# Kernel optimization log

Hardware: AMD Instinct MI355X
Metric: run time of the kernel (lower is better)

Reference implementation:

```python
import jax, jax.numpy as jnp
import numpy as np

N = 100000
E = 1600000
IN_C, HID_C, OUT_C = 64, 64, 16


def setup_inputs() -> dict:
    key = jax.random.key(0)
    k1, k2, k3, k4, k5 = jax.random.split(key, 5)
    x = jax.random.normal(k1, (N, IN_C), dtype=jnp.float32)
    edge_index = jax.random.randint(k2, (2, E), 0, N, dtype=jnp.int64)
    # Glorot-style init like PyG GCNConv
    W1 = jax.random.normal(k3, (IN_C, HID_C), dtype=jnp.float32) * (1.0 / np.sqrt(IN_C))
    b1 = jnp.zeros((HID_C,), dtype=jnp.float32)
    W2 = jax.random.normal(k4, (HID_C, OUT_C), dtype=jnp.float32) * (1.0 / np.sqrt(HID_C))
    b2 = jnp.zeros((OUT_C,), dtype=jnp.float32)
    return {"x": x, "edge_index": edge_index, "W1": W1, "b1": b1, "W2": W2, "b2": b2}


def _gcn_conv(h, src, dst, norm, W, b, n_nodes):
    # h: [N, F_in] -> linear transform first (PyG order), then normalized aggregation
    h = h @ W  # [N, F_out]
    msgs = h[src] * norm[:, None]          # gather + scale, [E+N, F_out]
    out = jax.ops.segment_sum(msgs, dst, num_segments=n_nodes)  # scatter-add
    return out + b


def reference(x, edge_index, W1, b1, W2, b2):
    n = x.shape[0]
    loop = jnp.arange(n, dtype=edge_index.dtype)
    src = jnp.concatenate([edge_index[0], loop])  # add self-loops
    dst = jnp.concatenate([edge_index[1], loop])
    # symmetric normalization D^{-1/2} (A+I) D^{-1/2}
    deg = jax.ops.segment_sum(jnp.ones_like(dst, dtype=x.dtype), dst, num_segments=n)
    dinv = jnp.where(deg > 0, jax.lax.rsqrt(deg), 0.0)
    norm = dinv[src] * dinv[dst]  # [E+N]

    h = jax.nn.relu(_gcn_conv(x, src, dst, norm, W1, b1, n))
    # dropout is identity in eval mode
    return _gcn_conv(h, src, dst, norm, W2, b2, n)
```

## Files before the change

kernel.cpp:

```cpp
#include <hip/hip_runtime.h>


namespace {
constexpr int BLK = 256;
constexpr int NPB = 256;
constexpr int PCHUNK = 8192;
constexpr int STRIDE = 5120;
constexpr int CPAD = 32;

__device__ inline float bf2f(unsigned short h) {
    union { unsigned u; float f; } v; v.u = (unsigned)h << 16; return v.f;
}
__device__ inline unsigned short f2bf(float f) {
    union { float f; unsigned u; } v; v.f = f;
    unsigned r = (v.u + 0x7FFFu + ((v.u >> 16) & 1u)) >> 16;
    return (unsigned short)r;
}
__device__ inline unsigned pack2bf(float a, float b) {
    return (unsigned)f2bf(a) | ((unsigned)f2bf(b) << 16);
}
__device__ inline int sel4(int s0, int s1, int s2, int s3, int q) {
    int sa = (q & 1) ? s1 : s0;
    int sb = (q & 1) ? s3 : s2;
    return (q & 2) ? sb : sa;
}

__device__ inline float gather8(const unsigned short* __restrict__ hhat,
                                const int* __restrict__ ssrc, int base, int lane) {
    int s0 = ssrc[base + 0], s1 = ssrc[base + 1];
    int s2 = ssrc[base + 2], s3 = ssrc[base + 3];
    int s4 = ssrc[base + 4], s5 = ssrc[base + 5];
    int s6 = ssrc[base + 6], s7 = ssrc[base + 7];
    float v0 = bf2f(hhat[((size_t)s0 << 6) + lane]);
    float v1 = bf2f(hhat[((size_t)s1 << 6) + lane]);
    float v2 = bf2f(hhat[((size_t)s2 << 6) + lane]);
    float v3 = bf2f(hhat[((size_t)s3 << 6) + lane]);
    float v4 = bf2f(hhat[((size_t)s4 << 6) + lane]);
    float v5 = bf2f(hhat[((size_t)s5 << 6) + lane]);
    float v6 = bf2f(hhat[((size_t)s6 << 6) + lane]);
    float v7 = bf2f(hhat[((size_t)s7 << 6) + lane]);
    return ((v0 + v1) + (v2 + v3)) + ((v4 + v5) + (v6 + v7));
}
__device__ inline float gather4(const unsigned short* __restrict__ hhat,
                                const int* __restrict__ ssrc, int base, int lane) {
    int s0 = ssrc[base + 0], s1 = ssrc[base + 1];
    int s2 = ssrc[base + 2], s3 = ssrc[base + 3];
    float v0 = bf2f(hhat[((size_t)s0 << 6) + lane]);
    float v1 = bf2f(hhat[((size_t)s1 << 6) + lane]);
    float v2 = bf2f(hhat[((size_t)s2 << 6) + lane]);
    float v3 = bf2f(hhat[((size_t)s3 << 6) + lane]);
    return (v0 + v1) + (v2 + v3);
}

__global__ __launch_bounds__(BLK) void k_part(const int* __restrict__ src,
                                              const int* __restrict__ dst,
                                              int* __restrict__ bcnt,
                                              unsigned* __restrict__ packed,
                                              int e, int nb) {
    __shared__ int hist[1024];
    __shared__ int base[1024];
    int t = threadIdx.x;
    int chunk0 = blockIdx.x * PCHUNK;
    if (chunk0 >= e) return;
    int lim = min(PCHUNK, e - chunk0);
    int lim4 = lim >> 2;
    for (int i = t; i < nb; i += BLK) hist[i] = 0;
    __syncthreads();
    const int4* d4 = (const int4*)(dst + chunk0);
    for (int i = t; i < lim4; i += BLK) {
        int4 d = d4[i];
        atomicAdd(&hist[d.x >> 8], 1);
        atomicAdd(&hist[d.y >> 8], 1);
        atomicAdd(&hist[d.z >> 8], 1);
        atomicAdd(&hist[d.w >> 8], 1);
    }
    for (int i = (lim4 << 2) + t; i < lim; i += BLK)
        atomicAdd(&hist[dst[chunk0 + i] >> 8], 1);
    __syncthreads();
    for (int i = t; i < nb; i += BLK) {
        int c = hist[i];
        base[i] = c ? (i * STRIDE + atomicAdd(&bcnt[i * CPAD], c)) : 0;
        hist[i] = 0;
    }
    __syncthreads();
    const int4* s4 = (const int4*)(src + chunk0);
    for (int i = t; i < lim4; i += BLK) {
        int4 d = d4[i];
        int4 s = s4[i];
        int b0 = d.x >> 8, b1 = d.y >> 8, b2 = d.z >> 8, b3 = d.w >> 8;
        int r0 = atomicAdd(&hist[b0], 1);
        packed[base[b0] + r0] = ((unsigned)s.x << 8) | (unsigned)(d.x & 255);
        int r1 = atomicAdd(&hist[b1], 1);
        packed[base[b1] + r1] = ((unsigned)s.y << 8) | (unsigned)(d.y & 255);
        int r2 = atomicAdd(&hist[b2], 1);
        packed[base[b2] + r2] = ((unsigned)s.z << 8) | (unsigned)(d.z & 255);
        int r3 = atomicAdd(&hist[b3], 1);
        packed[base[b3] + r3] = ((unsigned)s.w << 8) | (unsigned)(d.w & 255);
    }
    for (int i = (lim4 << 2) + t; i < lim; i += BLK) {
        int d = dst[chunk0 + i];
        int b = d >> 8;
        int r = atomicAdd(&hist[b], 1);
        packed[base[b] + r] = ((unsigned)src[chunk0 + i] << 8) | (unsigned)(d & 255);
    }
}

__global__ __launch_bounds__(BLK) void k_meta(const unsigned* __restrict__ packed,
                                              const int* __restrict__ bcnt,
                                              int* __restrict__ rowbeg,
                                              int* __restrict__ rowcnt,
                                              float* __restrict__ dinv, int n) {
    __shared__ int cnt[NPB];
    __shared__ int offs[NPB];
    int b = blockIdx.x;
    int t = threadIdx.x;
    int regionBase = b * STRIDE;
    int ecnt = bcnt[b * CPAD];
    cnt[t] = 0;
    __syncthreads();
    int e4 = ecnt >> 2;
    const uint4* p4 = (const uint4*)(packed + regionBase);
    for (int i = t; i < e4; i += BLK) {
        uint4 p = p4[i];
        atomicAdd(&cnt[p.x & 255u], 1);
        atomicAdd(&cnt[p.y & 255u], 1);
        atomicAdd(&cnt[p.z & 255u], 1);
        atomicAdd(&cnt[p.w & 255u], 1);
    }
    for (int i = (e4 << 2) + t; i < ecnt; i += BLK)
        atomicAdd(&cnt[packed[regionBase + i] & 255u], 1);
    __syncthreads();
    int v = cnt[t];
    offs[t] = v;
    __syncthreads();
    for (int off = 1; off < NPB; off <<= 1) {
        int x = (t >= off) ? offs[t - off] : 0;
        __syncthreads();
        offs[t] += x;
        __syncthreads();
    }
    int node = (b << 8) + t;
    if (node < n) {
        rowbeg[node] = regionBase + offs[t] - v;
        rowcnt[node] = v;
        dinv[node] = rsqrtf((float)(v + 1));
    }
}

union SMemU {
    int cnt[NPB];
    float W[64 * 64];
};

__global__ __launch_bounds__(BLK) void k_sortgemm(
    const unsigned* __restrict__ packed, const int* __restrict__ bcnt,
    const int* __restrict__ rowbeg, int* __restrict__ ssrc, int nsort, int n,
    const float* __restrict__ x, const float* __restrict__ W1,
    const float* __restrict__ dinv, unsigned short* __restrict__ hhat,
    int ntiles) {
    __shared__ SMemU sm;
    int t = threadIdx.x;
    if ((int)blockIdx.x < nsort) {
        int bid = blockIdx.x;
        int b = bid >> 1;
        int hf = bid & 1;
        int regionBase = b * STRIDE;
        int ecnt = bcnt[b * CPAD];
        int node = (b << 8) + t;
        sm.cnt[t] = (node < n) ? rowbeg[node] : 0;
        __syncthreads();
        int lo = hf << 7, hi = lo + 128;
        int e4 = ecnt >> 2;
        const uint4* p4 = (const uint4*)(packed + regionBase);
        for (int i = t; i < e4; i += BLK) {
            uint4 pp = p4[i];
            unsigned a[4] = {pp.x, pp.y, pp.z, pp.w};
            #pragma unroll
            for (int k = 0; k < 4; ++k) {
                int dl = (int)(a[k] & 255u);
                if (dl >= lo && dl < hi) {
                    int pos = atomicAdd(&sm.cnt[dl], 1);
                    ssrc[pos] = (int)(a[k] >> 8);
                }
            }
        }
        for (int i = (e4 << 2) + t; i < ecnt; i += BLK) {
            unsigned p = packed[regionBase + i];
            int dl = (int)(p & 255u);
            if (dl >= lo && dl < hi) {
                int pos = atomicAdd(&sm.cnt[dl], 1);
                ssrc[pos] = (int)(p >> 8);
            }
        }
    } else {
        #pragma unroll
        for (int i = 0; i < 16; ++i) sm.W[t + BLK * i] = W1[t + BLK * i];
        __syncthreads();
        const int cg = t & 3;
        const int ng = t >> 2;
        const float* Wc = sm.W + cg * 16;
        const int g1grid = gridDim.x - nsort;

        for (int tile = blockIdx.x - nsort; tile < ntiles; tile += g1grid) {
            const int node0 = tile * 256 + ng * 4;
            int nd[4];
            #pragma unroll
            for (int i = 0; i < 4; ++i) {
                int vv = node0 + i;
                nd[i] = (vv < n) ? vv : (n - 1);
            }
            float4 acc[4][4];
            #pragma unroll
            for (int i = 0; i < 4; ++i)
                #pragma unroll
                for (int c = 0; c < 4; ++c) acc[i][c] = make_float4(0.f, 0.f, 0.f, 0.f);

            for (int k4 = 0; k4 < 16; ++k4) {
                float4 xv[4];
                #pragma unroll
                for (int i = 0; i < 4; ++i)
                    xv[i] = ((const float4*)(x + (size_t)nd[i] * 64))[k4];
                #pragma unroll
                for (int kk = 0; kk < 4; ++kk) {
                    const float4* wr = (const float4*)(Wc + (k4 * 4 + kk) * 64);
                    float4 w0 = wr[0], w1 = wr[1], w2 = wr[2], w3 = wr[3];
                    #pragma unroll
                    for (int i = 0; i < 4; ++i) {
                        float xa[4] = {xv[i].x, xv[i].y, xv[i].z, xv[i].w};
                        float xs = xa[kk];
                        acc[i][0].x = fmaf(xs, w0.x, acc[i][0].x);
                        acc[i][0].y = fmaf(xs, w0.y, acc[i][0].y);
                        acc[i][0].z = fmaf(xs, w0.z, acc[i][0].z);
                        acc[i][0].w = fmaf(xs, w0.w, acc[i][0].w);
                        acc[i][1].x = fmaf(xs, w1.x, acc[i][1].x);
                        acc[i][1].y = fmaf(xs, w1.y, acc[i][1].y);
                        acc[i][1].z = fmaf(xs, w1.z, acc[i][1].z);
                        acc[i][1].w = fmaf(xs, w1.w, acc[i][1].w);
                        acc[i][2].x = fmaf(xs, w2.x, acc[i][2].x);
                        acc[i][2].y = fmaf(xs, w2.y, acc[i][2].y);
                        acc[i][2].z = fmaf(xs, w2.z, acc[i][2].z);
                        acc[i][2].w = fmaf(xs, w2.w, acc[i][2].w);
                        acc[i][3].x = fmaf(xs, w3.x, acc[i][3].x);
                        acc[i][3].y = fmaf(xs, w3.y, acc[i][3].y);
                        acc[i][3].z = fmaf(xs, w3.z, acc[i][3].z);
                        acc[i][3].w = fmaf(xs, w3.w, acc[i][3].w);
                    }
                }
            }
            #pragma unroll
            for (int i = 0; i < 4; ++i) {
                int vv = node0 + i;
                if (vv < n) {
                    float d = dinv[vv];
                    unsigned u0 = pack2bf(acc[i][0].x * d, acc[i][0].y * d);
                    unsigned u1 = pack2bf(acc[i][0].z * d, acc[i][0].w * d);
                    unsigned u2 = pack2bf(acc[i][1].x * d, acc[i][1].y * d);
                    unsigned u3 = pack2bf(acc[i][1].z * d, acc[i][1].w * d);
                    unsigned u4 = pack2bf(acc[i][2].x * d, acc[i][2].y * d);
                    unsigned u5 = pack2bf(acc[i][2].z * d, acc[i][2].w * d);
                    unsigned u6 = pack2bf(acc[i][3].x * d, acc[i][3].y * d);
                    unsigned u7 = pack2bf(acc[i][3].z * d, acc[i][3].w * d);
                    uint4* dstp = (uint4*)(hhat + (size_t)vv * 64 + cg * 16);
                    dstp[0] = make_uint4(u0, u1, u2, u3);
                    dstp[1] = make_uint4(u4, u5, u6, u7);
                }
            }
        }
    }
}


__global__ __launch_bounds__(BLK) void k_agg1(const unsigned short* __restrict__ hhat,
                                              const int* __restrict__ rowbeg,
                                              const int* __restrict__ rowcnt,
                                              const int* __restrict__ ssrc,
                                              const float* __restrict__ dinv,
                                              const float* __restrict__ b1,
                                              const float* __restrict__ W2,
                                              unsigned short* __restrict__ h2hat, int n) {
    int pair = __builtin_amdgcn_readfirstlane(
        (int)((blockIdx.x * BLK + threadIdx.x) >> 6));
    int lane = threadIdx.x & 63;
    int wid0 = pair << 1;
    if (wid0 >= n) return;
    int wid1 = wid0 + 1;
    bool has1 = (wid1 < n);
    const int g = lane >> 4;
    const int j = lane & 15;
    float w2r[16];
    #pragma unroll
    for (int k = 0; k < 16; ++k) w2r[k] = W2[(g * 16 + k) * 16 + j];

    int beg0 = rowbeg[wid0], cnt0 = rowcnt[wid0];
    int beg1 = 0, cnt1 = 0;
    if (has1) { beg1 = rowbeg[wid1]; cnt1 = rowcnt[wid1]; }
    float a0 = bf2f(hhat[((size_t)wid0 << 6) + lane]);
    float a1 = 0.f;
    if (has1) a1 = bf2f(hhat[((size_t)wid1 << 6) + lane]);
    int e0 = 0, e1 = 0;
    while (e0 + 8 <= cnt0 && e1 + 8 <= cnt1) {
        float r0 = gather8(hhat, ssrc, beg0 + e0, lane);
        float r1 = gather8(hhat, ssrc, beg1 + e1, lane);
        a0 += r0;
        a1 += r1;
        e0 += 8; e1 += 8;
    }
    for (; e0 + 8 <= cnt0; e0 += 8) a0 += gather8(hhat, ssrc, beg0 + e0, lane);
    for (; e1 + 8 <= cnt1; e1 += 8) a1 += gather8(hhat, ssrc, beg1 + e1, lane);
    if (e0 + 4 <= cnt0) { a0 += gather4(hhat, ssrc, beg0 + e0, lane); e0 += 4; }
    if (e1 + 4 <= cnt1) { a1 += gather4(hhat, ssrc, beg1 + e1, lane); e1 += 4; }
    for (; e0 < cnt0; ++e0) a0 += bf2f(hhat[((size_t)ssrc[beg0 + e0] << 6) + lane]);
    for (; e1 < cnt1; ++e1) a1 += bf2f(hhat[((size_t)ssrc[beg1 + e1] << 6) + lane]);

    {
        float dv = dinv[wid0];
        float h = fmaxf(fmaf(dv, a0, b1[lane]), 0.f);
        float part = 0.f;
        #pragma unroll
        for (int k = 0; k < 16; ++k)
            part = fmaf(__shfl(h, g * 16 + k, 64), w2r[k], part);
        part += __shfl_xor(part, 16, 64);
        part += __shfl_xor(part, 32, 64);
        if (g == 0) h2hat[(size_t)wid0 * 16 + j] = f2bf(part * dv);
    }
    if (has1) {
        float dv = dinv[wid1];
        float h = fmaxf(fmaf(dv, a1, b1[lane]), 0.f);
        float part = 0.f;
        #pragma unroll
        for (int k = 0; k < 16; ++k)
            part = fmaf(__shfl(h, g * 16 + k, 64), w2r[k], part);
        part += __shfl_xor(part, 16, 64);
        part += __shfl_xor(part, 32, 64);
        if (g == 0) h2hat[(size_t)wid1 * 16 + j] = f2bf(part * dv);
    }
}

__global__ __launch_bounds__(BLK) void k_agg2(const unsigned short* __restrict__ h2,
                                              const int* __restrict__ rowbeg,
                                              const int* __restrict__ rowcnt,
                                              const int* __restrict__ ssrc,
                                              const float* __restrict__ dinv,
                                              const float* __restrict__ b2,
                                              float* __restrict__ out, int n) {
    int pair = __builtin_amdgcn_readfirstlane(
        (int)((blockIdx.x * BLK + threadIdx.x) >> 6));
    int lane = threadIdx.x & 63;
    int w0 = pair << 1;
    if (w0 >= n) return;
    int w1 = w0 + 1;
    bool has1 = (w1 < n);
    int q = lane >> 4;
    int c = lane & 15;
    int beg0 = rowbeg[w0], cnt0 = rowcnt[w0];
    int beg1 = 0, cnt1 = 0;
    if (has1) { beg1 = rowbeg[w1]; cnt1 = rowcnt[w1]; }
    float a0 = 0.f, a1 = 0.f;
    int e0 = 0, e1 = 0;
    while (e0 + 8 <= cnt0 && e1 + 8 <= cnt1) {
        int p0 = beg0 + e0, p1 = beg1 + e1;
        int x0 = ssrc[p0 + 0], x1 = ssrc[p0 + 1], x2 = ssrc[p0 + 2], x3 = ssrc[p0 + 3];
        int x4 = ssrc[p0 + 4], x5 = ssrc[p0 + 5], x6 = ssrc[p0 + 6], x7 = ssrc[p0 + 7];
        int y0 = ssrc[p1 + 0], y1 = ssrc[p1 + 1], y2 = ssrc[p1 + 2], y3 = ssrc[p1 + 3];
        int y4 = ssrc[p1 + 4], y5 = ssrc[p1 + 5], y6 = ssrc[p1 + 6], y7 = ssrc[p1 + 7];
        int sA0 = sel4(x0, x1, x2, x3, q), sB0 = sel4(x4, x5, x6, x7, q);
        int sA1 = sel4(y0, y1, y2, y3, q), sB1 = sel4(y4, y5, y6, y7, q);
        float vA0 = bf2f(h2[((size_t)sA0 << 4) + c]);
        float vB0 = bf2f(h2[((size_t)sB0 << 4) + c]);
        float vA1 = bf2f(h2[((size_t)sA1 << 4) + c]);
        float vB1 = bf2f(h2[((size_t)sB1 << 4) + c]);
        a0 += vA0 + vB0;
        a1 += vA1 + vB1;
        e0 += 8; e1 += 8;
    }
    for (; e0 + 8 <= cnt0; e0 += 8) {
        int p0 = beg0 + e0;
        int x0 = ssrc[p0 + 0], x1 = ssrc[p0 + 1], x2 = ssrc[p0 + 2], x3 = ssrc[p0 + 3];
        int x4 = ssrc[p0 + 4], x5 = ssrc[p0 + 5], x6 = ssrc[p0 + 6], x7 = ssrc[p0 + 7];
        int sA = sel4(x0, x1, x2, x3, q), sB = sel4(x4, x5, x6, x7, q);
        a0 += bf2f(h2[((size_t)sA << 4) + c]) + bf2f(h2[((size_t)sB << 4) + c]);
    }
    if (e0 + 4 <= cnt0) {
        int p0 = beg0 + e0;
        int x0 = ssrc[p0 + 0], x1 = ssrc[p0 + 1], x2 = ssrc[p0 + 2], x3 = ssrc[p0 + 3];
        a0 += bf2f(h2[((size_t)sel4(x0, x1, x2, x3, q) << 4) + c]);
        e0 += 4;
    }
    if (e0 + q < cnt0)
        a0 += bf2f(h2[((size_t)ssrc[beg0 + e0 + q] << 4) + c]);
    for (; e1 + 8 <= cnt1; e1 += 8) {
        int p1 = beg1 + e1;
        int y0 = ssrc[p1 + 0], y1 = ssrc[p1 + 1], y2 = ssrc[p1 + 2], y3 = ssrc[p1 + 3];
        int y4 = ssrc[p1 + 4], y5 = ssrc[p1 + 5], y6 = ssrc[p1 + 6], y7 = ssrc[p1 + 7];
        int sA = sel4(y0, y1, y2, y3, q), sB = sel4(y4, y5, y6, y7, q);
        a1 += bf2f(h2[((size_t)sA << 4) + c]) + bf2f(h2[((size_t)sB << 4) + c]);
    }
    if (has1 && e1 + 4 <= cnt1) {
        int p1 = beg1 + e1;
        int y0 = ssrc[p1 + 0], y1 = ssrc[p1 + 1], y2 = ssrc[p1 + 2], y3 = ssrc[p1 + 3];
        a1 += bf2f(h2[((size_t)sel4(y0, y1, y2, y3, q) << 4) + c]);
        e1 += 4;
    }
    if (has1 && e1 + q < cnt1)
        a1 += bf2f(h2[((size_t)ssrc[beg1 + e1 + q] << 4) + c]);

    a0 += __shfl_xor(a0, 16, 64);
    a0 += __shfl_xor(a0, 32, 64);
    a1 += __shfl_xor(a1, 16, 64);
    a1 += __shfl_xor(a1, 32, 64);
    if (q == 0) {
        float self0 = bf2f(h2[((size_t)w0 << 4) + c]);
        out[((size_t)w0 << 4) + c] = fmaf(dinv[w0], a0 + self0, b2[c]);
        if (has1) {
            float self1 = bf2f(h2[((size_t)w1 << 4) + c]);
            out[((size_t)w1 << 4) + c] = fmaf(dinv[w1], a1 + self1, b2[c]);
        }
    }
}

}

extern "C" void kernel_launch(void* const* d_in, const int* in_sizes, int n_in,
                              void* d_out, int out_size, void* d_ws, size_t ws_size,
                              hipStream_t stream) {
    const float* x  = (const float*)d_in[0];
    const int*   ei = (const int*)d_in[1];
    const float* W1 = (const float*)d_in[2];
    const float* b1 = (const float*)d_in[3];
    const float* W2 = (const float*)d_in[4];
    const float* b2 = (const float*)d_in[5];
    float* out = (float*)d_out;

    const int N = in_sizes[0] / 64;
    const int E = in_sizes[1] / 2;
    const int* src = ei;
    const int* dst = ei + E;
    const int nb = (N + NPB - 1) / NPB;

    char* ws = (char*)d_ws;
    size_t off = 0;
    auto alloc = [&](size_t bytes) -> char* {
        char* p = ws + off;
        off = (off + bytes + 255) & ~(size_t)255;
        return p;
    };
    int*            bcnt   = (int*)alloc((size_t)1024 * CPAD * 4);
    int*            rowbeg = (int*)alloc((size_t)N * 4);
    int*            rowcnt = (int*)alloc((size_t)N * 4);
    float*          dinv   = (float*)alloc((size_t)N * 4);
    unsigned*       packed = (unsigned*)alloc((size_t)nb * STRIDE * 4);
    int*            ssrc   = (int*)alloc((size_t)nb * STRIDE * 4);
    unsigned short* hhat   = (unsigned short*)alloc((size_t)N * 64 * 2);
    unsigned short* h2hat  = (unsigned short*)alloc((size_t)N * 16 * 2);

    const int ntiles = (N + 255) / 256;
    const int g1grid = (ntiles < 1024) ? ntiles : 1024;
    const int nchunks = (E + PCHUNK - 1) / PCHUNK;
    const int npairs = (N + 1) / 2;
    const int nb_p = (int)(((long long)npairs * 64 + BLK - 1) / BLK);
    const int nsort = nb * 2;

    hipMemsetAsync(bcnt, 0, (size_t)nb * CPAD * 4, stream);
    k_part<<<nchunks, BLK, 0, stream>>>(src, dst, bcnt, packed, E, nb);
    k_meta<<<nb, BLK, 0, stream>>>(packed, bcnt, rowbeg, rowcnt, dinv, N);
    k_sortgemm<<<nsort + g1grid, BLK, 0, stream>>>(packed, bcnt, rowbeg, ssrc,
                                                   nsort, N, x, W1, dinv, hhat,
                                                   ntiles);
    k_agg1<<<nb_p, BLK, 0, stream>>>(hhat, rowbeg, rowcnt, ssrc, dinv, b1, W2,
                                     h2hat, N);
    k_agg2<<<nb_p, BLK, 0, stream>>>(h2hat, rowbeg, rowcnt, ssrc, dinv, b2, out, N);
}
```

Before: 201.1 us.

## Move layer-1 GEMM into partition kernel, defer dinv scaling to scatter kernel

Fuses the x@W1 GEMM blocks into the edge-partition launch instead of the sort launch, writing unscaled fp32 results to a new buffer. A separate pass in the scatter kernel then applies dinv and packs to bf16 once degrees are known. The aim is to overlap the GEMM with partitioning. In exchange it adds a full fp32 intermediate write and read.

```diff
diff --git a/kernel.cpp b/kernel.cpp
--- a/kernel.cpp
+++ b/kernel.cpp
@@ -52,145 +52,62 @@
     return (v0 + v1) + (v2 + v3);
 }
 
-__global__ __launch_bounds__(BLK) void k_part(const int* __restrict__ src,
-                                              const int* __restrict__ dst,
-                                              int* __restrict__ bcnt,
-                                              unsigned* __restrict__ packed,
-                                              int e, int nb) {
-    __shared__ int hist[1024];
-    __shared__ int base[1024];
-    int t = threadIdx.x;
-    int chunk0 = blockIdx.x * PCHUNK;
-    if (chunk0 >= e) return;
-    int lim = min(PCHUNK, e - chunk0);
-    int lim4 = lim >> 2;
-    for (int i = t; i < nb; i += BLK) hist[i] = 0;
-    __syncthreads();
-    const int4* d4 = (const int4*)(dst + chunk0);
-    for (int i = t; i < lim4; i += BLK) {
-        int4 d = d4[i];
-        atomicAdd(&hist[d.x >> 8], 1);
-        atomicAdd(&hist[d.y >> 8], 1);
-        atomicAdd(&hist[d.z >> 8], 1);
-        atomicAdd(&hist[d.w >> 8], 1);
-    }
-    for (int i = (lim4 << 2) + t; i < lim; i += BLK)
-        atomicAdd(&hist[dst[chunk0 + i] >> 8], 1);
-    __syncthreads();
-    for (int i = t; i < nb; i += BLK) {
-        int c = hist[i];
-        base[i] = c ? (i * STRIDE + atomicAdd(&bcnt[i * CPAD], c)) : 0;
-        hist[i] = 0;
-    }
-    __syncthreads();
-    const int4* s4 = (const int4*)(src + chunk0);
-    for (int i = t; i < lim4; i += BLK) {
-        int4 d = d4[i];
-        int4 s = s4[i];
-        int b0 = d.x >> 8, b1 = d.y >> 8, b2 = d.z >> 8, b3 = d.w >> 8;
-        int r0 = atomicAdd(&hist[b0], 1);
-        packed[base[b0] + r0] = ((unsigned)s.x << 8) | (unsigned)(d.x & 255);
-        int r1 = atomicAdd(&hist[b1], 1);
-        packed[base[b1] + r1] = ((unsigned)s.y << 8) | (unsigned)(d.y & 255);
-        int r2 = atomicAdd(&hist[b2], 1);
-        packed[base[b2] + r2] = ((unsigned)s.z << 8) | (unsigned)(d.z & 255);
-        int r3 = atomicAdd(&hist[b3], 1);
-        packed[base[b3] + r3] = ((unsigned)s.w << 8) | (unsigned)(d.w & 255);
-    }
-    for (int i = (lim4 << 2) + t; i < lim; i += BLK) {
-        int d = dst[chunk0 + i];
-        int b = d >> 8;
-        int r = atomicAdd(&hist[b], 1);
-        packed[base[b] + r] = ((unsigned)src[chunk0 + i] << 8) | (unsigned)(d & 255);
-    }
-}
-
-__global__ __launch_bounds__(BLK) void k_meta(const unsigned* __restrict__ packed,
-                                              const int* __restrict__ bcnt,
-                                              int* __restrict__ rowbeg,
-                                              int* __restrict__ rowcnt,
-                                              float* __restrict__ dinv, int n) {
-    __shared__ int cnt[NPB];
-    __shared__ int offs[NPB];
-    int b = blockIdx.x;
-    int t = threadIdx.x;
-    int regionBase = b * STRIDE;
-    int ecnt = bcnt[b * CPAD];
-    cnt[t] = 0;
-    __syncthreads();
-    int e4 = ecnt >> 2;
-    const uint4* p4 = (const uint4*)(packed + regionBase);
-    for (int i = t; i < e4; i += BLK) {
-        uint4 p = p4[i];
-        atomicAdd(&cnt[p.x & 255u], 1);
-        atomicAdd(&cnt[p.y & 255u], 1);
-        atomicAdd(&cnt[p.z & 255u], 1);
-        atomicAdd(&cnt[p.w & 255u], 1);
-    }
-    for (int i = (e4 << 2) + t; i < ecnt; i += BLK)
-        atomicAdd(&cnt[packed[regionBase + i] & 255u], 1);
-    __syncthreads();
-    int v = cnt[t];
-    offs[t] = v;
-    __syncthreads();
-    for (int off = 1; off < NPB; off <<= 1) {
-        int x = (t >= off) ? offs[t - off] : 0;
-        __syncthreads();
-        offs[t] += x;
-        __syncthreads();
-    }
-    int node = (b << 8) + t;
-    if (node < n) {
-        rowbeg[node] = regionBase + offs[t] - v;
-        rowcnt[node] = v;
-        dinv[node] = rsqrtf((float)(v + 1));
-    }
-}
-
-union SMemU {
-    int cnt[NPB];
+union SMemP {
+    struct { int hist[1024]; int base[1024]; } p;
     float W[64 * 64];
 };
 
-__global__ __launch_bounds__(BLK) void k_sortgemm(
-    const unsigned* __restrict__ packed, const int* __restrict__ bcnt,
-    const int* __restrict__ rowbeg, int* __restrict__ ssrc, int nsort, int n,
-    const float* __restrict__ x, const float* __restrict__ W1,
-    const float* __restrict__ dinv, unsigned short* __restrict__ hhat,
-    int ntiles) {
-    __shared__ SMemU sm;
+__global__ __launch_bounds__(BLK) void k_partgemm(
+    const int* __restrict__ src, const int* __restrict__ dst,
+    int* __restrict__ bcnt, unsigned* __restrict__ packed, int e, int nb,
+    int nchunks, const float* __restrict__ x, const float* __restrict__ W1,
+    float* __restrict__ h32, int n, int ntiles) {
+    __shared__ SMemP sm;
     int t = threadIdx.x;
-    if ((int)blockIdx.x < nsort) {
-        int bid = blockIdx.x;
-        int b = bid >> 1;
-        int hf = bid & 1;
-        int regionBase = b * STRIDE;
-        int ecnt = bcnt[b * CPAD];
-        int node = (b << 8) + t;
-        sm.cnt[t] = (node < n) ? rowbeg[node] : 0;
-        __syncthreads();
-        int lo = hf << 7, hi = lo + 128;
-        int e4 = ecnt >> 2;
-        const uint4* p4 = (const uint4*)(packed + regionBase);
-        for (int i = t; i < e4; i += BLK) {
-            uint4 pp = p4[i];
-            unsigned a[4] = {pp.x, pp.y, pp.z, pp.w};
-            #pragma unroll
-            for (int k = 0; k < 4; ++k) {
-                int dl = (int)(a[k] & 255u);
-                if (dl >= lo && dl < hi) {
-                    int pos = atomicAdd(&sm.cnt[dl], 1);
-                    ssrc[pos] = (int)(a[k] >> 8);
-                }
-            }
-        }
-        for (int i = (e4 << 2) + t; i < ecnt; i += BLK) {
-            unsigned p = packed[regionBase + i];
-            int dl = (int)(p & 255u);
-            if (dl >= lo && dl < hi) {
-                int pos = atomicAdd(&sm.cnt[dl], 1);
-                ssrc[pos] = (int)(p >> 8);
-            }
+    if ((int)blockIdx.x < nchunks) {
+        int chunk0 = blockIdx.x * PCHUNK;
+        if (chunk0 >= e) return;
+        int lim = min(PCHUNK, e - chunk0);
+        int lim4 = lim >> 2;
+        for (int i = t; i < nb; i += BLK) sm.p.hist[i] = 0;
+        __syncthreads();
+        const int4* d4 = (const int4*)(dst + chunk0);
+        for (int i = t; i < lim4; i += BLK) {
+            int4 d = d4[i];
+            atomicAdd(&sm.p.hist[d.x >> 8], 1);
+            atomicAdd(&sm.p.hist[d.y >> 8], 1);
+            atomicAdd(&sm.p.hist[d.z >> 8], 1);
+            atomicAdd(&sm.p.hist[d.w >> 8], 1);
+        }
+        for (int i = (lim4 << 2) + t; i < lim; i += BLK)
+            atomicAdd(&sm.p.hist[dst[chunk0 + i] >> 8], 1);
+        __syncthreads();
+        for (int i = t; i < nb; i += BLK) {
+            int c = sm.p.hist[i];
+            sm.p.base[i] = c ? (i * STRIDE + atomicAdd(&bcnt[i * CPAD], c)) : 0;
+            sm.p.hist[i] = 0;
+        }
+        __syncthreads();
+        const int4* s4 = (const int4*)(src + chunk0);
+        for (int i = t; i < lim4; i += BLK) {
+            int4 d = d4[i];
+            int4 s = s4[i];
+            int b0 = d.x >> 8, b1 = d.y >> 8, b2 = d.z >> 8, b3 = d.w >> 8;
+            int r0 = atomicAdd(&sm.p.hist[b0], 1);
+            packed[sm.p.base[b0] + r0] = ((unsigned)s.x << 8) | (unsigned)(d.x & 255);
+            int r1 = atomicAdd(&sm.p.hist[b1], 1);
+            packed[sm.p.base[b1] + r1] = ((unsigned)s.y << 8) | (unsigned)(d.y & 255);
+            int r2 = atomicAdd(&sm.p.hist[b2], 1);
+            packed[sm.p.base[b2] + r2] = ((unsigned)s.z << 8) | (unsigned)(d.z & 255);
+            int r3 = atomicAdd(&sm.p.hist[b3], 1);
+            packed[sm.p.base[b3] + r3] = ((unsigned)s.w << 8) | (unsigned)(d.w & 255);
+        }
+        for (int i = (lim4 << 2) + t; i < lim; i += BLK) {
+            int d = dst[chunk0 + i];
+            int b = d >> 8;
+            int r = atomicAdd(&sm.p.hist[b], 1);
+            packed[sm.p.base[b] + r] =
+                ((unsigned)src[chunk0 + i] << 8) | (unsigned)(d & 255);
         }
     } else {
         #pragma unroll
@@ -199,9 +116,9 @@
         const int cg = t & 3;
         const int ng = t >> 2;
         const float* Wc = sm.W + cg * 16;
-        const int g1grid = gridDim.x - nsort;
-
-        for (int tile = blockIdx.x - nsort; tile < ntiles; tile += g1grid) {
+        const int g1grid = gridDim.x - nchunks;
+
+        for (int tile = blockIdx.x - nchunks; tile < ntiles; tile += g1grid) {
             const int node0 = tile * 256 + ng * 4;
             int nd[4];
             #pragma unroll
@@ -251,19 +168,111 @@
             for (int i = 0; i < 4; ++i) {
                 int vv = node0 + i;
                 if (vv < n) {
-                    float d = dinv[vv];
-                    unsigned u0 = pack2bf(acc[i][0].x * d, acc[i][0].y * d);
-                    unsigned u1 = pack2bf(acc[i][0].z * d, acc[i][0].w * d);
-                    unsigned u2 = pack2bf(acc[i][1].x * d, acc[i][1].y * d);
-                    unsigned u3 = pack2bf(acc[i][1].z * d, acc[i][1].w * d);
-                    unsigned u4 = pack2bf(acc[i][2].x * d, acc[i][2].y * d);
-                    unsigned u5 = pack2bf(acc[i][2].z * d, acc[i][2].w * d);
-                    unsigned u6 = pack2bf(acc[i][3].x * d, acc[i][3].y * d);
-                    unsigned u7 = pack2bf(acc[i][3].z * d, acc[i][3].w * d);
-                    uint4* dstp = (uint4*)(hhat + (size_t)vv * 64 + cg * 16);
-                    dstp[0] = make_uint4(u0, u1, u2, u3);
-                    dstp[1] = make_uint4(u4, u5, u6, u7);
+                    float4* dstp = (float4*)(h32 + (size_t)vv * 64 + cg * 16);
+                    dstp[0] = acc[i][0];
+                    dstp[1] = acc[i][1];
+                    dstp[2] = acc[i][2];
+                    dstp[3] = acc[i][3];
                 }
+            }
+        }
+    }
+}
+
+__global__ __launch_bounds__(BLK) void k_meta(const unsigned* __restrict__ packed,
+                                              const int* __restrict__ bcnt,
+                                              int* __restrict__ rowbeg,
+                                              int* __restrict__ rowcnt,
+                                              float* __restrict__ dinv, int n) {
+    __shared__ int cnt[NPB];
+    __shared__ int offs[NPB];
+    int b = blockIdx.x;
+    int t = threadIdx.x;
+    int regionBase = b * STRIDE;
+    int ecnt = bcnt[b * CPAD];
+    cnt[t] = 0;
+    __syncthreads();
+    int e4 = ecnt >> 2;
+    const uint4* p4 = (const uint4*)(packed + regionBase);
+    for (int i = t; i < e4; i += BLK) {
+        uint4 p = p4[i];
+        atomicAdd(&cnt[p.x & 255u], 1);
+        atomicAdd(&cnt[p.y & 255u], 1);
+        atomicAdd(&cnt[p.z & 255u], 1);
+        atomicAdd(&cnt[p.w & 255u], 1);
+    }
+    for (int i = (e4 << 2) + t; i < ecnt; i += BLK)
+        atomicAdd(&cnt[packed[regionBase + i] & 255u], 1);
+    __syncthreads();
+    int v = cnt[t];
+    offs[t] = v;
+    __syncthreads();
+    for (int off = 1; off < NPB; off <<= 1) {
+        int x = (t >= off) ? offs[t - off] : 0;
+        __syncthreads();
+        offs[t] += x;
+        __syncthreads();
+    }
+    int node = (b << 8) + t;
+    if (node < n) {
+        rowbeg[node] = regionBase + offs[t] - v;
+        rowcnt[node] = v;
+        dinv[node] = rsqrtf((float)(v + 1));
+    }
+}
+
+__global__ __launch_bounds__(BLK) void k_scatterscale(
+    const unsigned* __restrict__ packed, const int* __restrict__ bcnt,
+    const int* __restrict__ rowbeg, int* __restrict__ ssrc, int nsort, int n,
+    const float* __restrict__ h32, const float* __restrict__ dinv,
+    unsigned short* __restrict__ hhat) {
+    __shared__ int cnt[NPB];
+    int t = threadIdx.x;
+    if ((int)blockIdx.x < nsort) {
+        int bid = blockIdx.x;
+        int b = bid >> 1;
+        int hf = bid & 1;
+        int regionBase = b * STRIDE;
+        int ecnt = bcnt[b * CPAD];
+        int node = (b << 8) + t;
+        cnt[t] = (node < n) ? rowbeg[node] : 0;
+        __syncthreads();
+        int lo = hf << 7, hi = lo + 128;
+        int e4 = ecnt >> 2;
+        const uint4* p4 = (const uint4*)(packed + regionBase);
+        for (int i = t; i < e4; i += BLK) {
+            uint4 pp = p4[i];
+            unsigned a[4] = {pp.x, pp.y, pp.z, pp.w};
+            #pragma unroll
+            for (int k = 0; k < 4; ++k) {
+                int dl = (int)(a[k] & 255u);
+                if (dl >= lo && dl < hi) {
+                    int pos = atomicAdd(&cnt[dl], 1);
+                    ssrc[pos] = (int)(a[k] >> 8);
+                }
+            }
+        }
+        for (int i = (e4 << 2) + t; i < ecnt; i += BLK) {
+            unsigned p = packed[regionBase + i];
+            int dl = (int)(p & 255u);
+            if (dl >= lo && dl < hi) {
+                int pos = atomicAdd(&cnt[dl], 1);
+                ssrc[pos] = (int)(p >> 8);
+            }
+        }
+    } else {
+        int sb = blockIdx.x - nsort;
+        int node0 = sb << 8;
+        const float2* h2p = (const float2*)h32;
+        unsigned* hh = (unsigned*)hhat;
+        #pragma unroll 4
+        for (int k = 0; k < 32; ++k) {
+            int i2 = t + k * BLK;
+            int node = node0 + (i2 >> 5);
+            if (node < n) {
+                float2 v = h2p[(size_t)node0 * 32 + i2];
+                float d = dinv[node];
+                hh[(size_t)node0 * 32 + i2] = pack2bf(v.x * d, v.y * d);
             }
         }
     }
@@ -450,6 +459,7 @@
     float*          dinv   = (float*)alloc((size_t)N * 4);
     unsigned*       packed = (unsigned*)alloc((size_t)nb * STRIDE * 4);
     int*            ssrc   = (int*)alloc((size_t)nb * STRIDE * 4);
+    float*          h32    = (float*)alloc((size_t)N * 64 * 4);
     unsigned short* hhat   = (unsigned short*)alloc((size_t)N * 64 * 2);
     unsigned short* h2hat  = (unsigned short*)alloc((size_t)N * 16 * 2);
 
@@ -461,11 +471,12 @@
     const int nsort = nb * 2;
 
     hipMemsetAsync(bcnt, 0, (size_t)nb * CPAD * 4, stream);
-    k_part<<<nchunks, BLK, 0, stream>>>(src, dst, bcnt, packed, E, nb);
+    k_partgemm<<<nchunks + g1grid, BLK, 0, stream>>>(src, dst, bcnt, packed, E,
+                                                     nb, nchunks, x, W1, h32,
+                                                     N, ntiles);
     k_meta<<<nb, BLK, 0, stream>>>(packed, bcnt, rowbeg, rowcnt, dinv, N);
-    k_sortgemm<<<nsort + g1grid, BLK, 0, stream>>>(packed, bcnt, rowbeg, ssrc,
-                                                   nsort, N, x, W1, dinv, hhat,
-                                                   ntiles);
+    k_scatterscale<<<nsort + nb, BLK, 0, stream>>>(packed, bcnt, rowbeg, ssrc,
+                                                   nsort, N, h32, dinv, hhat);
     k_agg1<<<nb_p, BLK, 0, stream>>>(hhat, rowbeg, rowcnt, ssrc, dinv, b1, W2,
                                      h2hat, N);
     k_agg2<<<nb_p, BLK, 0, stream>>>(h2hat, rowbeg, rowcnt, ssrc, dinv, b2, out, N);
```

After: 216.9 us. 1.08x slower.
